# Kernel optimization log

Hardware: AMD Instinct MI355X
Metric: run time of the kernel (lower is better)

Reference implementation:

```python
import jax, jax.numpy as jnp
import numpy as np

B, C_IN, L = 16, 64, 1024
HID, OUT, ORDER = 1024, 512, 4
EPS = 1e-5


def setup_inputs() -> dict:
    key = jax.random.key(0)
    ks = jax.random.split(key, 4)
    return {
        "x": jax.random.normal(ks[0], (B, C_IN, L), jnp.float32),
        "W_in": jax.random.normal(ks[1], (C_IN, HID), jnp.float32) / np.sqrt(C_IN).astype(np.float32),
        "b_in": jnp.zeros((HID,), jnp.float32),
        "coeffs1": jax.random.normal(ks[2], (HID, HID, ORDER), jnp.float32) * 0.01,
        "bias1": jnp.zeros((HID,), jnp.float32),
        "g1": jnp.ones((HID,), jnp.float32),
        "beta1": jnp.zeros((HID,), jnp.float32),
        "coeffs2": jax.random.normal(ks[3], (OUT, HID, ORDER), jnp.float32) * 0.01,
        "bias2": jnp.zeros((OUT,), jnp.float32),
        "g2": jnp.ones((OUT,), jnp.float32),
        "beta2": jnp.zeros((OUT,), jnp.float32),
    }


def _taylor_kan(x, coeffs, bias):
    # x: (B, L, C_in); coeffs: (out, C_in, order); y[b,l,o] = sum_i sum_c x^i * coeffs[o,c,i]
    # Expressed as order-wise GEMMs with a running power -- no (B,out,L,C) expand.
    order = coeffs.shape[-1]
    y = jnp.zeros(x.shape[:2] + (coeffs.shape[0],), x.dtype)
    xp = jnp.ones_like(x)  # x**0 (matches torch 0**0 == 1)
    for i in range(order):
        y = y + jnp.einsum('blc,oc->blo', xp, coeffs[:, :, i])
        if i + 1 < order:
            xp = xp * x
    return y + bias


def _layernorm(x, g, b):
    mu = jnp.mean(x, -1, keepdims=True)
    var = jnp.mean((x - mu) ** 2, -1, keepdims=True)
    return (x - mu) * jax.lax.rsqrt(var + EPS) * g + b


def reference(x, W_in, b_in, coeffs1, bias1, g1, beta1, coeffs2, bias2, g2, beta2):
    # x: (B, C_in, L) -> project channels to hidden: (B, L, HID)
    h = jnp.einsum('bcl,ch->blh', x, W_in) + b_in
    h = _taylor_kan(h, coeffs1, bias1)            # (B, L, HID)
    h = jax.nn.gelu(_layernorm(h, g1, beta1), approximate=False)
    h = _taylor_kan(h, coeffs2, bias2)            # (B, L, OUT)
    h = _layernorm(h, g2, beta2)
    return jnp.mean(h, axis=1)                    # adaptive avg pool over L -> (B, OUT)
```

## Files before the change

kernel.cpp:

```cpp
#include <hip/hip_runtime.h>
#include <math.h>

#define Bsz  16
#define CIN  64
#define LEN  1024
#define HIDN 1024
#define OUTN 512
#define MTOT (Bsz*LEN)
#define KTOT (3*HIDN)
#define LCHUNKS 32
#define LROWS   (LEN/LCHUNKS)

typedef __attribute__((ext_vector_type(8))) short bf16x8;
typedef __attribute__((ext_vector_type(16))) float f32x16;

__device__ __forceinline__ unsigned short f2bf(float x) {
    union { float f; unsigned int u; } v; v.f = x;
    unsigned int r = v.u + 0x7fff + ((v.u >> 16) & 1);
    return (unsigned short)(r >> 16);
}
__device__ __forceinline__ float bf2f(unsigned short u) {
    union { unsigned int u; float f; } v; v.u = ((unsigned int)u) << 16;
    return v.f;
}
__device__ __forceinline__ void gload_lds16(const void* g, void* l) {
    __builtin_amdgcn_global_load_lds((const __attribute__((address_space(1))) void*)g,
                                     (__attribute__((address_space(3))) void*)l, 16, 0, 0);
}

__global__ __launch_bounds__(256) void prep_w(const float* __restrict__ coeffs,
                                              const float* __restrict__ bias,
                                              unsigned short* __restrict__ WT,
                                              float* __restrict__ beff) {
    int o = blockIdx.x, t = threadIdx.x;
    float s = 0.f;
    unsigned short* wrow = WT + (size_t)o * KTOT;
    for (int c = t; c < HIDN; c += 256) {
        float4 v = *(const float4*)(coeffs + ((size_t)o * HIDN + c) * 4);
        s += v.x;
        wrow[c]            = f2bf(v.y);
        wrow[HIDN + c]     = f2bf(v.z);
        wrow[2 * HIDN + c] = f2bf(v.w);
    }
    __shared__ float red[4];
    for (int off = 32; off > 0; off >>= 1) s += __shfl_down(s, off, 64);
    if ((t & 63) == 0) red[t >> 6] = s;
    __syncthreads();
    if (t == 0) beff[o] = bias[o] + red[0] + red[1] + red[2] + red[3];
}

__global__ __launch_bounds__(256) void proj_in(const float* __restrict__ x,
                                               const float* __restrict__ Win,
                                               const float* __restrict__ bin,
                                               unsigned short* __restrict__ Hpow) {
    __shared__ float xs[CIN][17];
    int t = threadIdx.x;
    int m0 = blockIdx.x * 16;
    int b = m0 >> 10, l0 = m0 & 1023;
    for (int idx = t; idx < CIN * 16; idx += 256) {
        int c = idx >> 4, r = idx & 15;
        xs[c][r] = x[((size_t)b * CIN + c) * LEN + l0 + r];
    }
    __syncthreads();
    float acc[16][4];
#pragma unroll
    for (int r = 0; r < 16; r++)
#pragma unroll
        for (int j = 0; j < 4; j++) acc[r][j] = 0.f;
    for (int c = 0; c < CIN; c++) {
        float4 w = *(const float4*)(Win + (size_t)c * HIDN + 4 * t);
#pragma unroll
        for (int r = 0; r < 16; r++) {
            float xv = xs[c][r];
            acc[r][0] += xv * w.x; acc[r][1] += xv * w.y;
            acc[r][2] += xv * w.z; acc[r][3] += xv * w.w;
        }
    }
    float4 bb = *(const float4*)(bin + 4 * t);
    for (int r = 0; r < 16; r++) {
        unsigned short* dst = Hpow + (size_t)(m0 + r) * KTOT + 4 * t;
        float h0 = acc[r][0] + bb.x, h1 = acc[r][1] + bb.y;
        float h2 = acc[r][2] + bb.z, h3 = acc[r][3] + bb.w;
        ushort4 p1 = { f2bf(h0), f2bf(h1), f2bf(h2), f2bf(h3) };
        ushort4 p2 = { f2bf(h0*h0), f2bf(h1*h1), f2bf(h2*h2), f2bf(h3*h3) };
        ushort4 p3 = { f2bf(h0*h0*h0), f2bf(h1*h1*h1), f2bf(h2*h2*h2), f2bf(h3*h3*h3) };
        *(ushort4*)(dst)            = p1;
        *(ushort4*)(dst + HIDN)     = p2;
        *(ushort4*)(dst + 2*HIDN)   = p3;
    }
}

template<int N, bool BF16OUT>
__global__ __launch_bounds__(256) void mfma_gemm(const unsigned short* __restrict__ A,
                                                 const unsigned short* __restrict__ BT,
                                                 const float* __restrict__ beff,
                                                 void* __restrict__ Yv) {
    __shared__ unsigned short As[128 * 64];
    __shared__ unsigned short Bs[128 * 64];
    int t = threadIdx.x;
    int lane = t & 63, wave = t >> 6;
    int m0 = blockIdx.x * 128, n0 = blockIdx.y * 128;
    const unsigned short* Ab = A + (size_t)m0 * KTOT;
    const unsigned short* Bb = BT + (size_t)n0 * KTOT;

    int srow = lane >> 3;
    int sgcc = (lane & 7) ^ srow;

    f32x16 acc[2][2] = {};
    int wr = (wave >> 1) * 64;
    int wc = (wave & 1) * 64;
    int row32 = lane & 31, half = lane >> 5;

    for (int k0 = 0; k0 < KTOT; k0 += 64) {
#pragma unroll
        for (int j = 0; j < 4; j++) {
            int rgrp = wave * 32 + j * 8;
            gload_lds16(Ab + ((size_t)(rgrp + srow) * KTOT + k0 + sgcc * 8), As + rgrp * 64);
            gload_lds16(Bb + ((size_t)(rgrp + srow) * KTOT + k0 + sgcc * 8), Bs + rgrp * 64);
        }
        __syncthreads();
#pragma unroll
        for (int ks = 0; ks < 4; ks++) {
            int cidx = ks * 2 + half;
            bf16x8 af[2], bf[2];
#pragma unroll
            for (int mt = 0; mt < 2; mt++) {
                int r = wr + mt * 32 + row32;
                af[mt] = *(const bf16x8*)(As + r * 64 + ((cidx ^ (r & 7)) << 3));
            }
#pragma unroll
            for (int nt = 0; nt < 2; nt++) {
                int c = wc + nt * 32 + row32;
                bf[nt] = *(const bf16x8*)(Bs + c * 64 + ((cidx ^ (c & 7)) << 3));
            }
#pragma unroll
            for (int mt = 0; mt < 2; mt++)
#pragma unroll
                for (int nt = 0; nt < 2; nt++)
                    acc[mt][nt] = __builtin_amdgcn_mfma_f32_32x32x16_bf16(af[mt], bf[nt], acc[mt][nt], 0, 0, 0);
        }
        __syncthreads();
    }
#pragma unroll
    for (int nt = 0; nt < 2; nt++) {
        int oc = n0 + wc + nt * 32 + row32;
        float bo = beff[oc];
#pragma unroll
        for (int mt = 0; mt < 2; mt++) {
#pragma unroll
            for (int reg = 0; reg < 16; reg++) {
                int rl = (reg & 3) + 8 * (reg >> 2) + 4 * half;
                int mr = m0 + wr + mt * 32 + rl;
                float v = acc[mt][nt][reg] + bo;
                if (BF16OUT) ((unsigned short*)Yv)[(size_t)mr * N + oc] = f2bf(v);
                else         ((float*)Yv)[(size_t)mr * N + oc] = v;
            }
        }
    }
}

__global__ __launch_bounds__(256) void ln_gelu(const unsigned short* __restrict__ y1,
                                               const float* __restrict__ g,
                                               const float* __restrict__ be,
                                               unsigned short* __restrict__ Gpow) {
    __shared__ float red[4];
    int m = blockIdx.x, t = threadIdx.x;
    const unsigned short* row = y1 + (size_t)m * HIDN;
    ushort4 u = *(const ushort4*)(row + 4 * t);
    float v[4] = { bf2f(u.x), bf2f(u.y), bf2f(u.z), bf2f(u.w) };
    float s = v[0] + v[1] + v[2] + v[3];
    for (int off = 32; off > 0; off >>= 1) s += __shfl_down(s, off, 64);
    if ((t & 63) == 0) red[t >> 6] = s;
    __syncthreads();
    float mu = (red[0] + red[1] + red[2] + red[3]) * (1.f / HIDN);
    __syncthreads();
    float ss = 0.f;
#pragma unroll
    for (int j = 0; j < 4; j++) { float d = v[j] - mu; ss += d * d; }
    for (int off = 32; off > 0; off >>= 1) ss += __shfl_down(ss, off, 64);
    if ((t & 63) == 0) red[t >> 6] = ss;
    __syncthreads();
    float rs = rsqrtf((red[0] + red[1] + red[2] + red[3]) * (1.f / HIDN) + 1e-5f);
    float4 gg = *(const float4*)(g + 4 * t);
    float4 bb = *(const float4*)(be + 4 * t);
    float gl[4];
    float gv[4] = { gg.x, gg.y, gg.z, gg.w };
    float bv[4] = { bb.x, bb.y, bb.z, bb.w };
#pragma unroll
    for (int j = 0; j < 4; j++) {
        float xn = (v[j] - mu) * rs * gv[j] + bv[j];
        gl[j] = xn * 0.5f * (1.f + erff(xn * 0.70710678118654752f));
    }
    unsigned short* dst = Gpow + (size_t)m * KTOT + 4 * t;
    ushort4 p1 = { f2bf(gl[0]), f2bf(gl[1]), f2bf(gl[2]), f2bf(gl[3]) };
    ushort4 p2 = { f2bf(gl[0]*gl[0]), f2bf(gl[1]*gl[1]), f2bf(gl[2]*gl[2]), f2bf(gl[3]*gl[3]) };
    ushort4 p3 = { f2bf(gl[0]*gl[0]*gl[0]), f2bf(gl[1]*gl[1]*gl[1]),
                   f2bf(gl[2]*gl[2]*gl[2]), f2bf(gl[3]*gl[3]*gl[3]) };
    *(ushort4*)(dst)          = p1;
    *(ushort4*)(dst + HIDN)   = p2;
    *(ushort4*)(dst + 2*HIDN) = p3;
}

__global__ __launch_bounds__(256) void ln_pool_partial(const float* __restrict__ y2,
                                                       const float* __restrict__ g,
                                                       const float* __restrict__ be,
                                                       float* __restrict__ partial) {
    __shared__ float part[4][OUTN];
    int t = threadIdx.x, lane = t & 63, wave = t >> 6;
    int b = blockIdx.x, chunk = blockIdx.y;
    int mbase = b * LEN + chunk * LROWS;

    float4 gg0 = *(const float4*)(g + 4 * lane);
    float4 gg1 = *(const float4*)(g + 256 + 4 * lane);
    float4 bb0 = *(const float4*)(be + 4 * lane);
    float4 bb1 = *(const float4*)(be + 256 + 4 * lane);

    float acc[8] = {0.f, 0.f, 0.f, 0.f, 0.f, 0.f, 0.f, 0.f};
    for (int rr = wave; rr < LROWS; rr += 4) {
        const float* row = y2 + (size_t)(mbase + rr) * OUTN;
        float4 v0 = *(const float4*)(row + 4 * lane);
        float4 v1 = *(const float4*)(row + 256 + 4 * lane);
        float s  = v0.x + v0.y + v0.z + v0.w + v1.x + v1.y + v1.z + v1.w;
        float ss = v0.x*v0.x + v0.y*v0.y + v0.z*v0.z + v0.w*v0.w
                 + v1.x*v1.x + v1.y*v1.y + v1.z*v1.z + v1.w*v1.w;
        for (int off = 32; off > 0; off >>= 1) {
            s  += __shfl_down(s, off, 64);
            ss += __shfl_down(ss, off, 64);
        }
        s  = __shfl(s, 0, 64);
        ss = __shfl(ss, 0, 64);
        float mu = s * (1.f / OUTN);
        float var = ss * (1.f / OUTN) - mu * mu;
        float rs = rsqrtf(var + 1e-5f);
        acc[0] += (v0.x - mu) * rs * gg0.x + bb0.x;
        acc[1] += (v0.y - mu) * rs * gg0.y + bb0.y;
        acc[2] += (v0.z - mu) * rs * gg0.z + bb0.z;
        acc[3] += (v0.w - mu) * rs * gg0.w + bb0.w;
        acc[4] += (v1.x - mu) * rs * gg1.x + bb1.x;
        acc[5] += (v1.y - mu) * rs * gg1.y + bb1.y;
        acc[6] += (v1.z - mu) * rs * gg1.z + bb1.z;
        acc[7] += (v1.w - mu) * rs * gg1.w + bb1.w;
    }
    *(float4*)(&part[wave][4 * lane])       = *(float4*)(&acc[0]);
    *(float4*)(&part[wave][256 + 4 * lane]) = *(float4*)(&acc[4]);
    __syncthreads();
    float p0 = part[0][2*t] + part[1][2*t] + part[2][2*t] + part[3][2*t];
    float p1 = part[0][2*t+1] + part[1][2*t+1] + part[2][2*t+1] + part[3][2*t+1];
    float* dst = partial + ((size_t)b * LCHUNKS + chunk) * OUTN;
    *(float2*)(dst + 2 * t) = make_float2(p0, p1);
}

__global__ __launch_bounds__(256) void pool_reduce(const float* __restrict__ partial,
                                                   float* __restrict__ out) {
    int b = blockIdx.x, t = threadIdx.x;
    const float* src = partial + (size_t)b * LCHUNKS * OUTN;
    float s0 = 0.f, s1 = 0.f;
    for (int c = 0; c < LCHUNKS; c++) {
        float2 v = *(const float2*)(src + (size_t)c * OUTN + 2 * t);
        s0 += v.x; s1 += v.y;
    }
    *(float2*)(out + (size_t)b * OUTN + 2 * t) = make_float2(s0 * (1.f / LEN), s1 * (1.f / LEN));
}

extern "C" void kernel_launch(void* const* d_in, const int* in_sizes, int n_in,
                              void* d_out, int out_size, void* d_ws, size_t ws_size,
                              hipStream_t stream) {
    const float* x       = (const float*)d_in[0];
    const float* Win     = (const float*)d_in[1];
    const float* bin     = (const float*)d_in[2];
    const float* coeffs1 = (const float*)d_in[3];
    const float* bias1   = (const float*)d_in[4];
    const float* g1      = (const float*)d_in[5];
    const float* beta1   = (const float*)d_in[6];
    const float* coeffs2 = (const float*)d_in[7];
    const float* bias2   = (const float*)d_in[8];
    const float* g2      = (const float*)d_in[9];
    const float* beta2   = (const float*)d_in[10];
    float* out = (float*)d_out;

    char* ws = (char*)d_ws;
    unsigned short* Hpow = (unsigned short*)ws;
    char* p1 = ws + (size_t)MTOT * KTOT * 2;
    unsigned short* y1   = (unsigned short*)p1;
    float*          y2   = (float*)p1;
    char* p2 = p1 + (size_t)MTOT * HIDN * 2;
    unsigned short* W1T  = (unsigned short*)p2;
    char* p3 = p2 + (size_t)HIDN * KTOT * 2;
    unsigned short* W2T  = (unsigned short*)p3;
    char* p4 = p3 + (size_t)OUTN * KTOT * 2;
    float* b1e = (float*)p4;
    float* b2e = (float*)(p4 + HIDN * sizeof(float));
    unsigned short* G2pow = Hpow;
    float* partial = (float*)W1T;

    prep_w<<<HIDN, 256, 0, stream>>>(coeffs1, bias1, W1T, b1e);
    prep_w<<<OUTN, 256, 0, stream>>>(coeffs2, bias2, W2T, b2e);
    proj_in<<<MTOT / 16, 256, 0, stream>>>(x, Win, bin, Hpow);
    mfma_gemm<HIDN, true><<<dim3(MTOT / 128, HIDN / 128), 256, 0, stream>>>(Hpow, W1T, b1e, y1);
    ln_gelu<<<MTOT, 256, 0, stream>>>(y1, g1, beta1, G2pow);
    mfma_gemm<OUTN, false><<<dim3(MTOT / 128, OUTN / 128), 256, 0, stream>>>(G2pow, W2T, b2e, y2);
    ln_pool_partial<<<dim3(Bsz, LCHUNKS), 256, 0, stream>>>(y2, g2, beta2, partial);
    pool_reduce<<<Bsz, 256, 0, stream>>>(partial, out);
}
```

Measured before the change: 338.1 us.

## Replace scalar input projection with bf16 MFMA GEMM and merge prep kernels

```diff
diff --git a/kernel.cpp b/kernel.cpp
--- a/kernel.cpp
+++ b/kernel.cpp
@@ -28,65 +28,132 @@
                                      (__attribute__((address_space(3))) void*)l, 16, 0, 0);
 }
 
-__global__ __launch_bounds__(256) void prep_w(const float* __restrict__ coeffs,
-                                              const float* __restrict__ bias,
-                                              unsigned short* __restrict__ WT,
-                                              float* __restrict__ beff) {
-    int o = blockIdx.x, t = threadIdx.x;
-    float s = 0.f;
-    unsigned short* wrow = WT + (size_t)o * KTOT;
-    for (int c = t; c < HIDN; c += 256) {
-        float4 v = *(const float4*)(coeffs + ((size_t)o * HIDN + c) * 4);
-        s += v.x;
-        wrow[c]            = f2bf(v.y);
-        wrow[HIDN + c]     = f2bf(v.z);
-        wrow[2 * HIDN + c] = f2bf(v.w);
-    }
-    __shared__ float red[4];
-    for (int off = 32; off > 0; off >>= 1) s += __shfl_down(s, off, 64);
-    if ((t & 63) == 0) red[t >> 6] = s;
-    __syncthreads();
-    if (t == 0) beff[o] = bias[o] + red[0] + red[1] + red[2] + red[3];
-}
-
-__global__ __launch_bounds__(256) void proj_in(const float* __restrict__ x,
-                                               const float* __restrict__ Win,
-                                               const float* __restrict__ bin,
-                                               unsigned short* __restrict__ Hpow) {
-    __shared__ float xs[CIN][17];
-    int t = threadIdx.x;
-    int m0 = blockIdx.x * 16;
-    int b = m0 >> 10, l0 = m0 & 1023;
-    for (int idx = t; idx < CIN * 16; idx += 256) {
-        int c = idx >> 4, r = idx & 15;
-        xs[c][r] = x[((size_t)b * CIN + c) * LEN + l0 + r];
-    }
-    __syncthreads();
-    float acc[16][4];
-#pragma unroll
-    for (int r = 0; r < 16; r++)
-#pragma unroll
-        for (int j = 0; j < 4; j++) acc[r][j] = 0.f;
-    for (int c = 0; c < CIN; c++) {
-        float4 w = *(const float4*)(Win + (size_t)c * HIDN + 4 * t);
-#pragma unroll
-        for (int r = 0; r < 16; r++) {
-            float xv = xs[c][r];
-            acc[r][0] += xv * w.x; acc[r][1] += xv * w.y;
-            acc[r][2] += xv * w.z; acc[r][3] += xv * w.w;
-        }
-    }
-    float4 bb = *(const float4*)(bin + 4 * t);
-    for (int r = 0; r < 16; r++) {
-        unsigned short* dst = Hpow + (size_t)(m0 + r) * KTOT + 4 * t;
-        float h0 = acc[r][0] + bb.x, h1 = acc[r][1] + bb.y;
-        float h2 = acc[r][2] + bb.z, h3 = acc[r][3] + bb.w;
-        ushort4 p1 = { f2bf(h0), f2bf(h1), f2bf(h2), f2bf(h3) };
-        ushort4 p2 = { f2bf(h0*h0), f2bf(h1*h1), f2bf(h2*h2), f2bf(h3*h3) };
-        ushort4 p3 = { f2bf(h0*h0*h0), f2bf(h1*h1*h1), f2bf(h2*h2*h2), f2bf(h3*h3*h3) };
-        *(ushort4*)(dst)            = p1;
-        *(ushort4*)(dst + HIDN)     = p2;
-        *(ushort4*)(dst + 2*HIDN)   = p3;
+__global__ __launch_bounds__(256) void prep_all(const float* __restrict__ coeffs1,
+                                                const float* __restrict__ bias1,
+                                                const float* __restrict__ coeffs2,
+                                                const float* __restrict__ bias2,
+                                                const float* __restrict__ x,
+                                                const float* __restrict__ Win,
+                                                unsigned short* __restrict__ W1T,
+                                                float* __restrict__ b1e,
+                                                unsigned short* __restrict__ W2T,
+                                                float* __restrict__ b2e,
+                                                unsigned short* __restrict__ xT,
+                                                unsigned short* __restrict__ WinT) {
+    __shared__ float sm[64 * 65];
+    int bid = blockIdx.x, t = threadIdx.x;
+    if (bid < 1536) {
+        const float* coeffs; const float* bias; unsigned short* WT; float* beff; int o;
+        if (bid < 1024) { coeffs = coeffs1; bias = bias1; WT = W1T; beff = b1e; o = bid; }
+        else            { coeffs = coeffs2; bias = bias2; WT = W2T; beff = b2e; o = bid - 1024; }
+        float s = 0.f;
+        unsigned short* wrow = WT + (size_t)o * KTOT;
+        for (int c = t; c < HIDN; c += 256) {
+            float4 v = *(const float4*)(coeffs + ((size_t)o * HIDN + c) * 4);
+            s += v.x;
+            wrow[c]            = f2bf(v.y);
+            wrow[HIDN + c]     = f2bf(v.z);
+            wrow[2 * HIDN + c] = f2bf(v.w);
+        }
+        for (int off = 32; off > 0; off >>= 1) s += __shfl_down(s, off, 64);
+        if ((t & 63) == 0) sm[t >> 6] = s;
+        __syncthreads();
+        if (t == 0) beff[o] = bias[o] + sm[0] + sm[1] + sm[2] + sm[3];
+    } else {
+        const float* src; unsigned short* dstbase; size_t src_rstride;
+        int c0;
+        if (bid < 1792) {
+            int tile = bid - 1536; int b = tile >> 4; c0 = (tile & 15) * 64;
+            src = x + (size_t)b * CIN * LEN;  src_rstride = LEN;
+            dstbase = xT + ((size_t)b * LEN + c0) * CIN;
+        } else {
+            int tile = bid - 1792; c0 = tile * 64;
+            src = Win; src_rstride = HIDN;
+            dstbase = WinT + (size_t)c0 * CIN;
+        }
+#pragma unroll
+        for (int it = 0; it < 4; it++) {
+            int idx = t + it * 256;
+            int c = idx >> 4, q = idx & 15;
+            float4 v = *(const float4*)(src + (size_t)c * src_rstride + c0 + q * 4);
+            sm[c * 65 + q * 4 + 0] = v.x;
+            sm[c * 65 + q * 4 + 1] = v.y;
+            sm[c * 65 + q * 4 + 2] = v.z;
+            sm[c * 65 + q * 4 + 3] = v.w;
+        }
+        __syncthreads();
+        int ll = t >> 2, cg = (t & 3) * 16;
+        unsigned short* dst = dstbase + (size_t)ll * CIN + cg;
+#pragma unroll
+        for (int j = 0; j < 4; j++) {
+            int c = cg + j * 4;
+            ushort4 w = { f2bf(sm[(c + 0) * 65 + ll]), f2bf(sm[(c + 1) * 65 + ll]),
+                          f2bf(sm[(c + 2) * 65 + ll]), f2bf(sm[(c + 3) * 65 + ll]) };
+            *(ushort4*)(dst + j * 4) = w;
+        }
+    }
+}
+
+__global__ __launch_bounds__(256) void proj_mfma(const unsigned short* __restrict__ xT,
+                                                 const unsigned short* __restrict__ WinT,
+                                                 const float* __restrict__ bin,
+                                                 unsigned short* __restrict__ Hpow) {
+    __shared__ unsigned short As[128 * 64];
+    __shared__ unsigned short Bs[128 * 64];
+    int t = threadIdx.x, lane = t & 63, wave = t >> 6;
+    int m0 = blockIdx.x * 128, n0 = blockIdx.y * 128;
+    int srow = lane >> 3, sgcc = (lane & 7) ^ srow;
+    const unsigned short* Ab = xT + (size_t)m0 * CIN;
+    const unsigned short* Bb = WinT + (size_t)n0 * CIN;
+
+    f32x16 acc[2][2] = {};
+    int wr = (wave >> 1) * 64, wc = (wave & 1) * 64;
+    int row32 = lane & 31, half = lane >> 5;
+
+#pragma unroll
+    for (int j = 0; j < 4; j++) {
+        int rgrp = wave * 32 + j * 8;
+        gload_lds16(Ab + (size_t)(rgrp + srow) * CIN + sgcc * 8, As + rgrp * 64);
+        gload_lds16(Bb + (size_t)(rgrp + srow) * CIN + sgcc * 8, Bs + rgrp * 64);
+    }
+    __syncthreads();
+#pragma unroll
+    for (int ks = 0; ks < 4; ks++) {
+        int cidx = ks * 2 + half;
+        bf16x8 af[2], bf[2];
+#pragma unroll
+        for (int mt = 0; mt < 2; mt++) {
+            int r = wr + mt * 32 + row32;
+            af[mt] = *(const bf16x8*)(As + r * 64 + ((cidx ^ (r & 7)) << 3));
+        }
+#pragma unroll
+        for (int nt = 0; nt < 2; nt++) {
+            int c = wc + nt * 32 + row32;
+            bf[nt] = *(const bf16x8*)(Bs + c * 64 + ((cidx ^ (c & 7)) << 3));
+        }
+#pragma unroll
+        for (int mt = 0; mt < 2; mt++)
+#pragma unroll
+            for (int nt = 0; nt < 2; nt++)
+                acc[mt][nt] = __builtin_amdgcn_mfma_f32_32x32x16_bf16(af[mt], bf[nt], acc[mt][nt], 0, 0, 0);
+    }
+#pragma unroll
+    for (int nt = 0; nt < 2; nt++) {
+        int oc = n0 + wc + nt * 32 + row32;
+        float bo = bin[oc];
+#pragma unroll
+        for (int mt = 0; mt < 2; mt++) {
+#pragma unroll
+            for (int reg = 0; reg < 16; reg++) {
+                int rl = (reg & 3) + 8 * (reg >> 2) + 4 * half;
+                size_t mr = (size_t)(m0 + wr + mt * 32 + rl);
+                float h = acc[mt][nt][reg] + bo;
+                unsigned short* d = Hpow + mr * KTOT + oc;
+                d[0]        = f2bf(h);
+                d[HIDN]     = f2bf(h * h);
+                d[2 * HIDN] = f2bf(h * h * h);
+            }
+        }
     }
 }
 
@@ -290,12 +357,16 @@
     char* p4 = p3 + (size_t)OUTN * KTOT * 2;
     float* b1e = (float*)p4;
     float* b2e = (float*)(p4 + HIDN * sizeof(float));
+    char* p5 = p4 + (HIDN + OUTN) * sizeof(float);
+    unsigned short* xT   = (unsigned short*)p5;
+    char* p6 = p5 + (size_t)MTOT * CIN * 2;
+    unsigned short* WinT = (unsigned short*)p6;
     unsigned short* G2pow = Hpow;
     float* partial = (float*)W1T;
 
-    prep_w<<<HIDN, 256, 0, stream>>>(coeffs1, bias1, W1T, b1e);
-    prep_w<<<OUTN, 256, 0, stream>>>(coeffs2, bias2, W2T, b2e);
-    proj_in<<<MTOT / 16, 256, 0, stream>>>(x, Win, bin, Hpow);
+    prep_all<<<1808, 256, 0, stream>>>(coeffs1, bias1, coeffs2, bias2, x, Win,
+                                       W1T, b1e, W2T, b2e, xT, WinT);
+    proj_mfma<<<dim3(MTOT / 128, HIDN / 128), 256, 0, stream>>>(xT, WinT, bin, Hpow);
     mfma_gemm<HIDN, true><<<dim3(MTOT / 128, HIDN / 128), 256, 0, stream>>>(Hpow, W1T, b1e, y1);
     ln_gelu<<<MTOT, 256, 0, stream>>>(y1, g1, beta1, G2pow);
     mfma_gemm<OUTN, false><<<dim3(MTOT / 128, OUTN / 128), 256, 0, stream>>>(G2pow, W2T, b2e, y2);
```

After: 314.5 us. -7.0%, faster.
